# Kernel tuning notes

Measured on AMD Instinct MI355X. Metric: run time of the kernel, lower is better.

Reference implementation:

```python
import jax, jax.numpy as jnp
import numpy as np

NUM_NEURONS = 10000
D = 784
BATCH = 4096


def setup_inputs() -> dict:
    key = jax.random.key(0)
    kx, kw = jax.random.split(key)
    x = jax.random.normal(kx, (BATCH, D), dtype=jnp.float32)
    weights = jax.random.normal(kw, (NUM_NEURONS, D), dtype=jnp.float32)
    return {"x": x, "weights": weights}


def reference(x, weights):
    # SOM BMU lookup: squared distances between each input row and every
    # codebook row, argmin over the codebook, gather the winning neuron.
    # Use |a|^2 + |b|^2 - 2ab to avoid the (B, N, D) broadcast intermediate.
    x = x.reshape(-1, D)  # (B, D)
    x_sq = jnp.sum(x * x, axis=1, keepdims=True)          # (B, 1)
    w_sq = jnp.sum(weights * weights, axis=1)             # (N,)
    cross = x @ weights.T                                 # (B, N) GEMM
    distances = x_sq + w_sq[None, :] - 2.0 * cross        # (B, N)
    bmu_indices = jnp.argmin(distances, axis=1)           # (B,)
    bmu = jnp.take(weights, bmu_indices, axis=0)          # (B, D)
    return bmu
```

## Files before the change

### kernel.cpp

```cpp
#include <hip/hip_runtime.h>
#include <math.h>

#define BATCH 4096
#define D 784
#define N 10000

#define KP 800
#define BK 32
#define KT (KP / BK)
#define BM 128
#define BN 128
#define GXMAX 80
#define NPAD (GXMAX * BN)
#define MARGIN 3.0f

typedef __attribute__((ext_vector_type(8))) short bh8;
typedef __attribute__((ext_vector_type(4))) float fx4;
typedef const __attribute__((address_space(1))) void CGV;
typedef __attribute__((address_space(3))) void LDSV;

static __device__ __forceinline__ unsigned short f2bf(float f) {
    unsigned u = __float_as_uint(f);
    unsigned r = u + 0x7fffu + ((u >> 16) & 1u);
    return (unsigned short)(r >> 16);
}

static __device__ __forceinline__ void top2_insert(float w, int j, float& v0, int& i0,
                                                   float& v1, int& i1) {
    if (w < v0 || (w == v0 && j < i0)) { v1 = v0; i1 = i0; v0 = w; i0 = j; }
    else if (w < v1 || (w == v1 && j < i1)) { v1 = w; i1 = j; }
}

__global__ __launch_bounds__(256) void convert_x_kernel(const float* __restrict__ x,
                                                        unsigned short* __restrict__ xh) {
    int row = blockIdx.x;
    const float4* xr = (const float4*)(x + (size_t)row * D);
    unsigned short* dst = xh + (size_t)row * KP;
    for (int i = threadIdx.x; i < KP / 4; i += 256) {
        int k = i * 4;
        uint2 o;
        if (k < D) {
            float4 v = xr[i];
            o.x = (unsigned)f2bf(v.x) | ((unsigned)f2bf(v.y) << 16);
            o.y = (unsigned)f2bf(v.z) | ((unsigned)f2bf(v.w) << 16);
        } else { o.x = 0u; o.y = 0u; }
        *(uint2*)(dst + k) = o;
    }
}

__global__ __launch_bounds__(256) void convert_w_kernel(const float* __restrict__ w,
                                                        unsigned short* __restrict__ wh,
                                                        float* __restrict__ wsq) {
    int row = blockIdx.x;
    unsigned short* dst = wh + (size_t)row * KP;
    float s = 0.f;
    if (row < N) {
        const float4* wr = (const float4*)(w + (size_t)row * D);
        for (int i = threadIdx.x; i < KP / 4; i += 256) {
            int k = i * 4;
            uint2 o;
            if (k < D) {
                float4 v = wr[i];
                s += v.x * v.x + v.y * v.y + v.z * v.z + v.w * v.w;
                o.x = (unsigned)f2bf(v.x) | ((unsigned)f2bf(v.y) << 16);
                o.y = (unsigned)f2bf(v.z) | ((unsigned)f2bf(v.w) << 16);
            } else { o.x = 0u; o.y = 0u; }
            *(uint2*)(dst + k) = o;
        }
    } else {
        for (int i = threadIdx.x; i < KP / 4; i += 256) {
            uint2 o; o.x = 0u; o.y = 0u;
            *(uint2*)(dst + i * 4) = o;
        }
    }
    __shared__ float sred[4];
    #pragma unroll
    for (int off = 32; off; off >>= 1) s += __shfl_down(s, off);
    if ((threadIdx.x & 63) == 0) sred[threadIdx.x >> 6] = s;
    __syncthreads();
    if (threadIdx.x == 0) {
        float t = sred[0] + sred[1] + sred[2] + sred[3];
        wsq[row] = (row < N) ? t : INFINITY;
    }
}

__global__ __launch_bounds__(256, 4) void dist_mfma_kernel(
    const unsigned short* __restrict__ xh, const unsigned short* __restrict__ wh,
    const float* __restrict__ wsq, float4* __restrict__ partial,
    int gx, int cpb) {
    __shared__ __align__(16) unsigned short As[2][BM * BK];
    __shared__ __align__(16) unsigned short Bs[2][BN * BK];
    __shared__ float4 red[BM][2];

    const int tid = threadIdx.x;
    const int lane = tid & 63;
    const int wid = tid >> 6;
    const int waveM = (wid >> 1) * 64;
    const int waveN = (wid & 1) * 64;

    const int L = blockIdx.x + gx * blockIdx.y;
    const int xcd = L & 7;
    const int s = L >> 3;
    const int bx = s >> 2;
    const int by = xcd * 4 + (s & 3);
    const int rowBase = by * BM;
    const int colBase0 = bx * (cpb * BN);

    const int rr = tid >> 2;
    const int csw = (tid & 3) ^ ((rr >> 1) & 3);
    const unsigned short* aSrc0 = xh + (size_t)(rowBase + rr) * KP + csw * 8;
    const unsigned short* aSrc1 = aSrc0 + (size_t)64 * KP;

    char* ldsA0 = (char*)&As[0][0] + wid * 1024;
    char* ldsA1 = (char*)&As[1][0] + wid * 1024;
    char* ldsB0 = (char*)&Bs[0][0] + wid * 1024;
    char* ldsB1 = (char*)&Bs[1][0] + wid * 1024;

    int offA[4], offB[4];
    #pragma unroll
    for (int m = 0; m < 4; m++) {
        int r = waveM + m * 16 + (lane & 15);
        offA[m] = r * BK + (((lane >> 4) ^ ((r >> 1) & 3)) << 3);
    }
    #pragma unroll
    for (int n = 0; n < 4; n++) {
        int r = waveN + n * 16 + (lane & 15);
        offB[n] = r * BK + (((lane >> 4) ^ ((r >> 1) & 3)) << 3);
    }

    float V0[16], V1[16];
    int I0[16], I1[16];
    #pragma unroll
    for (int q = 0; q < 16; q++) {
        V0[q] = INFINITY; V1[q] = INFINITY;
        I0[q] = 0x7fffffff; I1[q] = 0x7fffffff;
    }

#define STAGE(nb, k0)                                                                  \
    do {                                                                               \
        __builtin_amdgcn_global_load_lds((CGV*)(aSrc0 + (k0)), (LDSV*)(ldsA##nb), 16, 0, 0);        \
        __builtin_amdgcn_global_load_lds((CGV*)(aSrc1 + (k0)), (LDSV*)(ldsA##nb + 4096), 16, 0, 0); \
        __builtin_amdgcn_global_load_lds((CGV*)(bSrc0 + (k0)), (LDSV*)(ldsB##nb), 16, 0, 0);        \
        __builtin_amdgcn_global_load_lds((CGV*)(bSrc1 + (k0)), (LDSV*)(ldsB##nb + 4096), 16, 0, 0); \
    } while (0)

#define COMPUTE(nb)                                                                    \
    do {                                                                               \
        bh8 af[4], bf[4];                                                              \
        _Pragma("unroll")                                                              \
        for (int m = 0; m < 4; m++) af[m] = *(const bh8*)&As[nb][offA[m]];             \
        _Pragma("unroll")                                                              \
        for (int n = 0; n < 4; n++) bf[n] = *(const bh8*)&Bs[nb][offB[n]];             \
        _Pragma("unroll")                                                              \
        for (int m = 0; m < 4; m++)                                                    \
            _Pragma("unroll")                                                          \
            for (int n = 0; n < 4; n++)                                                \
                acc[m][n] = __builtin_amdgcn_mfma_f32_16x16x32_bf16(af[m], bf[n],      \
                                                                    acc[m][n], 0, 0, 0); \
    } while (0)

#define VM0 asm volatile("s_waitcnt vmcnt(0)" ::: "memory")
#define BARR __builtin_amdgcn_s_barrier()

    #pragma unroll 1
    for (int c = 0; c < cpb; ++c) {
        const int colBase = colBase0 + c * BN;
        const unsigned short* bSrc0 = wh + (size_t)(colBase + rr) * KP + csw * 8;
        const unsigned short* bSrc1 = bSrc0 + (size_t)64 * KP;

        fx4 acc[4][4];
        #pragma unroll
        for (int m = 0; m < 4; m++)
            #pragma unroll
            for (int n = 0; n < 4; n++) acc[m][n] = (fx4)0.f;

        STAGE(0, 0);
        VM0; BARR;
        #pragma unroll 1
        for (int t = 0; t < KT - 1; t += 2) {
            STAGE(1, (t + 1) * BK);
            COMPUTE(0);
            VM0; BARR;
            STAGE(0, (t + 2) * BK);
            COMPUTE(1);
            VM0; BARR;
        }
        COMPUTE(0);

        const int cb = colBase + waveN + (lane & 15);
        #pragma unroll
        for (int n = 0; n < 4; n++) {
            const float wq = wsq[cb + n * 16];
            const int ci = cb + n * 16;
            #pragma unroll
            for (int m = 0; m < 4; m++)
                #pragma unroll
                for (int r = 0; r < 4; r++) {
                    float dv = wq - 2.f * acc[m][n][r];
                    top2_insert(dv, ci, V0[m * 4 + r], I0[m * 4 + r],
                                V1[m * 4 + r], I1[m * 4 + r]);
                }
        }
        __syncthreads();
    }

#undef STAGE
#undef COMPUTE
#undef VM0
#undef BARR

    #pragma unroll
    for (int q = 0; q < 16; q++) {
        float v0 = V0[q], v1 = V1[q];
        int i0 = I0[q], i1 = I1[q];
        #pragma unroll
        for (int mask = 1; mask < 16; mask <<= 1) {
            float w0 = __shfl_xor(v0, mask); int j0 = __shfl_xor(i0, mask);
            float w1 = __shfl_xor(v1, mask); int j1 = __shfl_xor(i1, mask);
            top2_insert(w0, j0, v0, i0, v1, i1);
            top2_insert(w1, j1, v0, i0, v1, i1);
        }
        if ((lane & 15) == 0) {
            int m = q >> 2, r = q & 3;
            int row_local = waveM + m * 16 + (lane >> 4) * 4 + r;
            red[row_local][wid & 1] =
                make_float4(v0, __int_as_float(i0), v1, __int_as_float(i1));
        }
    }
    __syncthreads();
    if (tid < BM) {
        float4 pa = red[tid][0], pb = red[tid][1];
        float v0 = pa.x, v1 = pa.z;
        int i0 = __float_as_int(pa.y), i1 = __float_as_int(pa.w);
        top2_insert(pb.x, __float_as_int(pb.y), v0, i0, v1, i1);
        top2_insert(pb.z, __float_as_int(pb.w), v0, i0, v1, i1);
        partial[(size_t)(rowBase + tid) * gx + bx] =
            make_float4(v0, __int_as_float(i0), v1, __int_as_float(i1));
    }
}

__global__ __launch_bounds__(256) void rescore_kernel(const float* __restrict__ x,
                                                      const float* __restrict__ w,
                                                      const float4* __restrict__ partial,
                                                      float* __restrict__ out, int ng) {
    int wid = threadIdx.x >> 6, lane = threadIdx.x & 63;
    int row = blockIdx.x * 4 + wid;
    __shared__ int s_cnt[4];
    __shared__ int s_cand[4][64];

    const float4* part = partial + (size_t)row * ng;

    float bv = INFINITY;
    for (int c = lane; c < ng; c += 64) bv = fminf(bv, part[c].x);
    #pragma unroll
    for (int mask = 1; mask < 64; mask <<= 1) bv = fminf(bv, __shfl_xor(bv, mask));
    float thr = bv + MARGIN;

    if (lane == 0) s_cnt[wid] = 0;
    __syncthreads();
    for (int c = lane; c < ng; c += 64) {
        float4 p = part[c];
        if (p.x <= thr) {
            int pos = atomicAdd(&s_cnt[wid], 1);
            if (pos < 64) s_cand[wid][pos] = __float_as_int(p.y);
        }
        if (p.z <= thr) {
            int pos = atomicAdd(&s_cnt[wid], 1);
            if (pos < 64) s_cand[wid][pos] = __float_as_int(p.w);
        }
    }
    __syncthreads();
    int cnt = s_cnt[wid]; if (cnt > 64) cnt = 64;

    double bd = INFINITY; int bi = 0x7fffffff;
    for (int c = 0; c < cnt; c++) {
        int idx = s_cand[wid][c];
        const float* wr = w + (size_t)idx * D;
        const float* xr = x + (size_t)row * D;
        double s = 0.0;
        for (int d = lane; d < D; d += 64) {
            double wv = (double)wr[d];
            s += wv * (wv - 2.0 * (double)xr[d]);
        }
        #pragma unroll
        for (int mask = 1; mask < 64; mask <<= 1) s += __shfl_xor(s, mask);
        if (s < bd || (s == bd && idx < bi)) { bd = s; bi = idx; }
    }

    const float4* src = (const float4*)(w + (size_t)bi * D);
    float4* dst = (float4*)(out + (size_t)row * D);
    for (int i = lane; i < D / 4; i += 64) dst[i] = src[i];
}

extern "C" void kernel_launch(void* const* d_in, const int* in_sizes, int n_in,
                              void* d_out, int out_size, void* d_ws, size_t ws_size,
                              hipStream_t stream) {
    const float* x = (const float*)d_in[0];
    const float* w = (const float*)d_in[1];
    float* out = (float*)d_out;

    const size_t off_xh = 0;
    const size_t off_wh = off_xh + (size_t)BATCH * KP * 2;
    const size_t off_wsq = off_wh + (size_t)NPAD * KP * 2;
    const size_t off_part = off_wsq + (size_t)NPAD * 4;

    int gx = 80, cpb = 1;
    if (ws_size < off_part + (size_t)BATCH * 80 * 16) { gx = 40; cpb = 2; }
    if (ws_size < off_part + (size_t)BATCH * 40 * 16) { gx = 20; cpb = 4; }

    unsigned short* xh = (unsigned short*)((char*)d_ws + off_xh);
    unsigned short* wh = (unsigned short*)((char*)d_ws + off_wh);
    float* wsq = (float*)((char*)d_ws + off_wsq);
    float4* partial = (float4*)((char*)d_ws + off_part);

    hipLaunchKernelGGL(convert_x_kernel, dim3(BATCH), dim3(256), 0, stream, x, xh);
    hipLaunchKernelGGL(convert_w_kernel, dim3(NPAD), dim3(256), 0, stream, w, wh, wsq);
    hipLaunchKernelGGL(dist_mfma_kernel, dim3(gx, 32), dim3(256), 0, stream,
                       xh, wh, wsq, partial, gx, cpb);
    hipLaunchKernelGGL(rescore_kernel, dim3(BATCH / 4), dim3(256), 0, stream,
                       x, w, partial, out, gx);
}
```

Baseline: 570.8 us.

## Reduce top-2 per column tile in-loop and fix grid to two column tiles per block

The per-thread top-2 register arrays (V0/V1/I0/I1, 64 registers) are removed. Instead, each column tile's results are reduced across lanes immediately and written to a shared-memory buffer indexed by tile, then merged once at the end. The workspace-size-dependent grid choice is replaced by a fixed 40 x 32 grid with two column tiles per block, and launch bounds drop from 4 to 2 blocks per CU. This cuts register pressure and the partial-result volume for the rescore pass, at the cost of a shuffle reduction per column tile and possibly lower occupancy.

```diff
diff --git a/kernel.cpp b/kernel.cpp
--- a/kernel.cpp
+++ b/kernel.cpp
@@ -10,8 +10,9 @@
 #define KT (KP / BK)
 #define BM 128
 #define BN 128
-#define GXMAX 80
-#define NPAD (GXMAX * BN)
+#define CPB 2
+#define NG 40
+#define NPAD (NG * 256)
 #define MARGIN 3.0f
 
 typedef __attribute__((ext_vector_type(8))) short bh8;
@@ -84,13 +85,12 @@
     }
 }
 
-__global__ __launch_bounds__(256, 4) void dist_mfma_kernel(
+__global__ __launch_bounds__(256, 2) void dist_mfma_kernel(
     const unsigned short* __restrict__ xh, const unsigned short* __restrict__ wh,
-    const float* __restrict__ wsq, float4* __restrict__ partial,
-    int gx, int cpb) {
+    const float* __restrict__ wsq, float4* __restrict__ partial) {
     __shared__ __align__(16) unsigned short As[2][BM * BK];
     __shared__ __align__(16) unsigned short Bs[2][BN * BK];
-    __shared__ float4 red[BM][2];
+    __shared__ float4 red[BM][2][CPB];
 
     const int tid = threadIdx.x;
     const int lane = tid & 63;
@@ -98,13 +98,13 @@
     const int waveM = (wid >> 1) * 64;
     const int waveN = (wid & 1) * 64;
 
-    const int L = blockIdx.x + gx * blockIdx.y;
+    const int L = blockIdx.x + NG * blockIdx.y;
     const int xcd = L & 7;
     const int s = L >> 3;
     const int bx = s >> 2;
     const int by = xcd * 4 + (s & 3);
     const int rowBase = by * BM;
-    const int colBase0 = bx * (cpb * BN);
+    const int colBase0 = bx * (CPB * BN);
 
     const int rr = tid >> 2;
     const int csw = (tid & 3) ^ ((rr >> 1) & 3);
@@ -126,14 +126,6 @@
     for (int n = 0; n < 4; n++) {
         int r = waveN + n * 16 + (lane & 15);
         offB[n] = r * BK + (((lane >> 4) ^ ((r >> 1) & 3)) << 3);
-    }
-
-    float V0[16], V1[16];
-    int I0[16], I1[16];
-    #pragma unroll
-    for (int q = 0; q < 16; q++) {
-        V0[q] = INFINITY; V1[q] = INFINITY;
-        I0[q] = 0x7fffffff; I1[q] = 0x7fffffff;
     }
 
 #define STAGE(nb, k0)                                                                  \
@@ -159,11 +151,8 @@
                                                                     acc[m][n], 0, 0, 0); \
     } while (0)
 
-#define VM0 asm volatile("s_waitcnt vmcnt(0)" ::: "memory")
-#define BARR __builtin_amdgcn_s_barrier()
-
     #pragma unroll 1
-    for (int c = 0; c < cpb; ++c) {
+    for (int c = 0; c < CPB; ++c) {
         const int colBase = colBase0 + c * BN;
         const unsigned short* bSrc0 = wh + (size_t)(colBase + rr) * KP + csw * 8;
         const unsigned short* bSrc1 = bSrc0 + (size_t)64 * KP;
@@ -175,66 +164,67 @@
             for (int n = 0; n < 4; n++) acc[m][n] = (fx4)0.f;
 
         STAGE(0, 0);
-        VM0; BARR;
+        asm volatile("s_waitcnt vmcnt(0)" ::: "memory");
+        __builtin_amdgcn_s_barrier();
         #pragma unroll 1
         for (int t = 0; t < KT - 1; t += 2) {
             STAGE(1, (t + 1) * BK);
             COMPUTE(0);
-            VM0; BARR;
+            asm volatile("s_waitcnt vmcnt(0)" ::: "memory");
+            __builtin_amdgcn_s_barrier();
             STAGE(0, (t + 2) * BK);
             COMPUTE(1);
-            VM0; BARR;
+            asm volatile("s_waitcnt vmcnt(0)" ::: "memory");
+            __builtin_amdgcn_s_barrier();
         }
         COMPUTE(0);
 
         const int cb = colBase + waveN + (lane & 15);
         #pragma unroll
-        for (int n = 0; n < 4; n++) {
-            const float wq = wsq[cb + n * 16];
-            const int ci = cb + n * 16;
+        for (int m = 0; m < 4; m++) {
             #pragma unroll
-            for (int m = 0; m < 4; m++)
+            for (int r = 0; r < 4; r++) {
+                float v0 = INFINITY, v1 = INFINITY;
+                int i0 = 0x7fffffff, i1 = 0x7fffffff;
                 #pragma unroll
-                for (int r = 0; r < 4; r++) {
-                    float dv = wq - 2.f * acc[m][n][r];
-                    top2_insert(dv, ci, V0[m * 4 + r], I0[m * 4 + r],
-                                V1[m * 4 + r], I1[m * 4 + r]);
+                for (int n = 0; n < 4; n++) {
+                    float dv = wsq[cb + n * 16] - 2.f * acc[m][n][r];
+                    top2_insert(dv, cb + n * 16, v0, i0, v1, i1);
                 }
+                #pragma unroll
+                for (int mask = 1; mask < 16; mask <<= 1) {
+                    float w0 = __shfl_xor(v0, mask); int j0 = __shfl_xor(i0, mask);
+                    float w1 = __shfl_xor(v1, mask); int j1 = __shfl_xor(i1, mask);
+                    top2_insert(w0, j0, v0, i0, v1, i1);
+                    top2_insert(w1, j1, v0, i0, v1, i1);
+                }
+                if ((lane & 15) == 0) {
+                    int row_local = waveM + m * 16 + (lane >> 4) * 4 + r;
+                    red[row_local][wid & 1][c] =
+                        make_float4(v0, __int_as_float(i0), v1, __int_as_float(i1));
+                }
+            }
         }
         __syncthreads();
     }
 
 #undef STAGE
 #undef COMPUTE
-#undef VM0
-#undef BARR
-
-    #pragma unroll
-    for (int q = 0; q < 16; q++) {
-        float v0 = V0[q], v1 = V1[q];
-        int i0 = I0[q], i1 = I1[q];
+
+    if (tid < BM) {
+        float4 p0 = red[tid][0][0];
+        float v0 = p0.x, v1 = p0.z;
+        int i0 = __float_as_int(p0.y), i1 = __float_as_int(p0.w);
         #pragma unroll
-        for (int mask = 1; mask < 16; mask <<= 1) {
-            float w0 = __shfl_xor(v0, mask); int j0 = __shfl_xor(i0, mask);
-            float w1 = __shfl_xor(v1, mask); int j1 = __shfl_xor(i1, mask);
-            top2_insert(w0, j0, v0, i0, v1, i1);
-            top2_insert(w1, j1, v0, i0, v1, i1);
-        }
-        if ((lane & 15) == 0) {
-            int m = q >> 2, r = q & 3;
-            int row_local = waveM + m * 16 + (lane >> 4) * 4 + r;
-            red[row_local][wid & 1] =
-                make_float4(v0, __int_as_float(i0), v1, __int_as_float(i1));
-        }
-    }
-    __syncthreads();
-    if (tid < BM) {
-        float4 pa = red[tid][0], pb = red[tid][1];
-        float v0 = pa.x, v1 = pa.z;
-        int i0 = __float_as_int(pa.y), i1 = __float_as_int(pa.w);
-        top2_insert(pb.x, __float_as_int(pb.y), v0, i0, v1, i1);
-        top2_insert(pb.z, __float_as_int(pb.w), v0, i0, v1, i1);
-        partial[(size_t)(rowBase + tid) * gx + bx] =
+        for (int h = 0; h < 2; h++)
+            #pragma unroll
+            for (int c = 0; c < CPB; c++) {
+                if (h == 0 && c == 0) continue;
+                float4 p = red[tid][h][c];
+                top2_insert(p.x, __float_as_int(p.y), v0, i0, v1, i1);
+                top2_insert(p.z, __float_as_int(p.w), v0, i0, v1, i1);
+            }
+        partial[(size_t)(rowBase + tid) * NG + bx] =
             make_float4(v0, __int_as_float(i0), v1, __int_as_float(i1));
     }
 }
@@ -304,10 +294,6 @@
     const size_t off_wsq = off_wh + (size_t)NPAD * KP * 2;
     const size_t off_part = off_wsq + (size_t)NPAD * 4;
 
-    int gx = 80, cpb = 1;
-    if (ws_size < off_part + (size_t)BATCH * 80 * 16) { gx = 40; cpb = 2; }
-    if (ws_size < off_part + (size_t)BATCH * 40 * 16) { gx = 20; cpb = 4; }
-
     unsigned short* xh = (unsigned short*)((char*)d_ws + off_xh);
     unsigned short* wh = (unsigned short*)((char*)d_ws + off_wh);
     float* wsq = (float*)((char*)d_ws + off_wsq);
@@ -315,8 +301,8 @@
 
     hipLaunchKernelGGL(convert_x_kernel, dim3(BATCH), dim3(256), 0, stream, x, xh);
     hipLaunchKernelGGL(convert_w_kernel, dim3(NPAD), dim3(256), 0, stream, w, wh, wsq);
-    hipLaunchKernelGGL(dist_mfma_kernel, dim3(gx, 32), dim3(256), 0, stream,
-                       xh, wh, wsq, partial, gx, cpb);
+    hipLaunchKernelGGL(dist_mfma_kernel, dim3(NG, 32), dim3(256), 0, stream,
+                       xh, wh, wsq, partial);
     hipLaunchKernelGGL(rescore_kernel, dim3(BATCH / 4), dim3(256), 0, stream,
-                       x, w, partial, out, gx);
-}
+                       x, w, partial, out, NG);
+}
```

Measured after the change: 489.3 us. 1.17x faster.
